# Performance work log

Measured on AMD Instinct MI355X. Metric: run time of the kernel, lower is better.

Reference implementation:

```python
import jax, jax.numpy as jnp
import numpy as np

D_IN = 1024
D_OUT = 1024
NUM_HEADS = 16
HEAD_DIM = D_OUT // NUM_HEADS
WINDOW = 256


def setup_inputs() -> dict:
    key = jax.random.key(0)
    ks = jax.random.split(key, 6)
    s = 0.02
    x = jax.random.normal(ks[0], (2, 2048, D_IN), dtype=jnp.float32)
    Wq = jax.random.normal(ks[1], (D_IN, D_OUT), dtype=jnp.float32) * s
    Wk = jax.random.normal(ks[2], (D_IN, D_OUT), dtype=jnp.float32) * s
    Wv = jax.random.normal(ks[3], (D_IN, D_OUT), dtype=jnp.float32) * s
    Wo = jax.random.normal(ks[4], (D_OUT, D_OUT), dtype=jnp.float32) * s
    bo = jnp.zeros((D_OUT,), dtype=jnp.float32)
    return {"x": x, "Wq": Wq, "Wk": Wk, "Wv": Wv, "Wo": Wo, "bo": bo}


def reference(x, Wq, Wk, Wv, Wo, bo):
    b, s, _ = x.shape
    # project and split heads: [b, h, s, hd]
    def heads(t):
        return t.reshape(b, s, NUM_HEADS, HEAD_DIM).transpose(0, 2, 1, 3)
    q = heads(x @ Wq)
    k = heads(x @ Wk)
    v = heads(x @ Wv)
    scores = jnp.einsum('bhqd,bhkd->bhqk', q, k) / jnp.sqrt(jnp.float32(HEAD_DIM))
    # symmetric sliding-window band: |i - j| <= WINDOW
    i = jnp.arange(s)
    band = jnp.abs(i[:, None] - i[None, :]) <= WINDOW  # [s, s]
    scores = jnp.where(band[None, None], scores, -jnp.inf)
    probs = jax.nn.softmax(scores, axis=-1)  # dropout=0.0 -> identity
    ctx = jnp.einsum('bhqk,bhkd->bhqd', probs, v)
    ctx = ctx.transpose(0, 2, 1, 3).reshape(b, s, D_OUT)
    return ctx @ Wo + bo
```

## Files before the change

kernel.cpp:

```cpp
#include <hip/hip_runtime.h>
#include <hip/hip_bf16.h>

typedef __bf16 bf16_t;
typedef __bf16 bf16x8 __attribute__((ext_vector_type(8)));
typedef __bf16 bf16x4 __attribute__((ext_vector_type(4)));
typedef float  f32x4  __attribute__((ext_vector_type(4)));

#define SEQ    2048
#define BATCH  2
#define NHEAD  16
#define HDIM   64
#define DMODEL 1024
#define WIN    256

__device__ __forceinline__ void async_load16(const void* g, void* l) {
    __builtin_amdgcn_global_load_lds(
        (const __attribute__((address_space(1))) char*)(uintptr_t)g,
        (__attribute__((address_space(3))) char*)(uintptr_t)l, 16, 0, 0);
}

__global__ void cast_x_kernel(const float* __restrict__ x, bf16_t* __restrict__ xb, int n4) {
    int i = blockIdx.x * blockDim.x + threadIdx.x;
    if (i >= n4) return;
    float4 v = ((const float4*)x)[i];
    bf16x4 o;
    o[0] = (bf16_t)v.x; o[1] = (bf16_t)v.y; o[2] = (bf16_t)v.z; o[3] = (bf16_t)v.w;
    ((bf16x4*)xb)[i] = o;
}

__global__ void transpose_w_kernel(const float* __restrict__ Wq, const float* __restrict__ Wk,
                                   const float* __restrict__ Wv, const float* __restrict__ Wo,
                                   bf16_t* __restrict__ Wt) {
    __shared__ float tile[32][33];
    const float* W = (blockIdx.z == 0) ? Wq : (blockIdx.z == 1) ? Wk : (blockIdx.z == 2) ? Wv : Wo;
    bf16_t* out = Wt + (size_t)blockIdx.z * DMODEL * DMODEL;
    int k0 = blockIdx.y * 32, n0 = blockIdx.x * 32;
    int tx = threadIdx.x, ty = threadIdx.y;
#pragma unroll
    for (int i = 0; i < 4; i++)
        tile[ty + i * 8][tx] = W[(size_t)(k0 + ty + i * 8) * DMODEL + n0 + tx];
    __syncthreads();
#pragma unroll
    for (int i = 0; i < 4; i++)
        out[(size_t)(n0 + ty + i * 8) * DMODEL + k0 + tx] = (bf16_t)tile[tx][ty + i * 8];
}

template <int EPI>
__global__ __launch_bounds__(256) void gemm_bt_kernel(
    const bf16_t* __restrict__ A, const bf16_t* __restrict__ Bt,
    bf16_t* __restrict__ Qb, bf16_t* __restrict__ Kb, bf16_t* __restrict__ Vt,
    float* __restrict__ Out, const float* __restrict__ bo, int K) {
    __shared__ __attribute__((aligned(16))) bf16_t As[128 * 64];
    __shared__ __attribute__((aligned(16))) bf16_t Bs[128 * 64];
    const int tid = threadIdx.x;
    const int wave = tid >> 6, lane = tid & 63, quad = lane >> 4, l15 = lane & 15;
    const int wm = wave >> 1, wn = wave & 1;
    const int m0 = blockIdx.y * 128, n0 = blockIdx.x * 128;

    f32x4 acc[4][4] = {};

    for (int kt = 0; kt < K; kt += 64) {
#pragma unroll
        for (int i = 0; i < 4; i++) {
            int v = tid + i * 256;
            int row = v >> 3, c = (v & 7) ^ (row & 7);
            async_load16(A + (size_t)(m0 + row) * K + kt + c * 8, (char*)As + (size_t)v * 16);
            async_load16(Bt + (size_t)(n0 + row) * K + kt + c * 8, (char*)Bs + (size_t)v * 16);
        }
        __syncthreads();
#pragma unroll
        for (int kk = 0; kk < 64; kk += 32) {
            bf16x8 am[4], bn[4];
#pragma unroll
            for (int i = 0; i < 4; i++) {
                int row = wm * 64 + i * 16 + l15;
                int ch = ((kk >> 3) + quad) ^ (row & 7);
                am[i] = *(const bf16x8*)&As[row * 64 + ch * 8];
            }
#pragma unroll
            for (int j = 0; j < 4; j++) {
                int row = wn * 64 + j * 16 + l15;
                int ch = ((kk >> 3) + quad) ^ (row & 7);
                bn[j] = *(const bf16x8*)&Bs[row * 64 + ch * 8];
            }
#pragma unroll
            for (int i = 0; i < 4; i++)
#pragma unroll
                for (int j = 0; j < 4; j++)
                    acc[i][j] = __builtin_amdgcn_mfma_f32_16x16x32_bf16(am[i], bn[j], acc[i][j], 0, 0, 0);
        }
        __syncthreads();
    }

#pragma unroll
    for (int i = 0; i < 4; i++)
#pragma unroll
        for (int j = 0; j < 4; j++)
#pragma unroll
            for (int r = 0; r < 4; r++) {
                int mg = m0 + wm * 64 + i * 16 + quad * 4 + r;
                int ng = n0 + wn * 64 + j * 16 + l15;
                float v = acc[i][j][r];
                if (EPI == 0) {
                    int sel = ng >> 10, nl = ng & 1023, h = nl >> 6, d = nl & 63;
                    int b = mg >> 11, s = mg & 2047;
                    size_t idx = ((size_t)((b * NHEAD + h) * SEQ) + s) * HDIM + d;
                    if (sel == 0)      Qb[idx] = (bf16_t)(v * 0.125f);
                    else if (sel == 1) Kb[idx] = (bf16_t)v;
                    else               Vt[((size_t)((b * NHEAD + h) * HDIM) + d) * SEQ + s] = (bf16_t)v;
                } else {
                    Out[(size_t)mg * DMODEL + ng] = v + bo[ng];
                }
            }
}

__global__ __launch_bounds__(256) void attn_kernel(
    const bf16_t* __restrict__ Qb, const bf16_t* __restrict__ Kb,
    const bf16_t* __restrict__ Vt, bf16_t* __restrict__ ctx) {
    __shared__ __attribute__((aligned(16))) bf16_t Ks[2][64 * 64];
    __shared__ __attribute__((aligned(16))) bf16_t Vs[2][64 * 64];
    __shared__ __attribute__((aligned(16))) bf16_t Plds[4][16][72];
    const int tid = threadIdx.x;
    const int wave = tid >> 6, lane = tid & 63, quad = lane >> 4, l15 = lane & 15;

    const int id = blockIdx.x;
    const int task = (id & 7) * 128 + (id >> 3);
    const int b = task >> 9, h = (task >> 5) & 15, q0 = (task & 31) << 6;
    const int qbase = q0 + wave * 16;

    const bf16_t* Qp = Qb + (size_t)(b * NHEAD + h) * SEQ * HDIM;
    const bf16_t* Kp = Kb + (size_t)(b * NHEAD + h) * SEQ * HDIM;
    const bf16_t* Vp = Vt + (size_t)(b * NHEAD + h) * HDIM * SEQ;

    bf16x8 qa0 = *(const bf16x8*)(Qp + (size_t)(qbase + l15) * HDIM + quad * 8);
    bf16x8 qa1 = *(const bf16x8*)(Qp + (size_t)(qbase + l15) * HDIM + 32 + quad * 8);

    bf16x8 ones;
#pragma unroll
    for (int j = 0; j < 8; j++) ones[j] = (bf16_t)1.0f;

    f32x4 O[4] = {};
    f32x4 lacc = {};

    const int qt = q0 >> 6;
    const int t0 = (qt - 4 > 0) ? qt - 4 : 0;
    const int t1 = (qt + 4 < SEQ / 64 - 1) ? qt + 4 : SEQ / 64 - 1;

    auto stage = [&](int kt, int buf) {
        const int k0 = kt * 64;
#pragma unroll
        for (int i = 0; i < 2; i++) {
            int v = tid + i * 256;
            int row = v >> 3, c = (v & 7) ^ (row & 7);
            async_load16(Kp + (size_t)(k0 + row) * HDIM + c * 8, (char*)&Ks[buf][0] + (size_t)v * 16);
            async_load16(Vp + (size_t)row * SEQ + k0 + c * 8, (char*)&Vs[buf][0] + (size_t)v * 16);
        }
    };

    stage(t0, 0);
    int cb = 0;
    for (int kt = t0; kt <= t1; kt++) {
        __syncthreads();
        if (kt < t1) stage(kt + 1, cb ^ 1);
        const int k0 = kt * 64;
        f32x4 s[4];
#pragma unroll
        for (int c = 0; c < 4; c++) {
            int row = c * 16 + l15;
            bf16x8 kb0 = *(const bf16x8*)&Ks[cb][row * 64 + (quad ^ (row & 7)) * 8];
            bf16x8 kb1 = *(const bf16x8*)&Ks[cb][row * 64 + ((quad + 4) ^ (row & 7)) * 8];
            f32x4 a = {};
            a = __builtin_amdgcn_mfma_f32_16x16x32_bf16(qa0, kb0, a, 0, 0, 0);
            a = __builtin_amdgcn_mfma_f32_16x16x32_bf16(qa1, kb1, a, 0, 0, 0);
            s[c] = a;
        }
        const int dt = kt - qt;
        const bool edge = (dt <= -4 || dt >= 4);
#pragma unroll
        for (int c = 0; c < 4; c++)
#pragma unroll
            for (int r = 0; r < 4; r++) {
                float sv = s[c][r];
                if (edge) {
                    int i = qbase + quad * 4 + r;
                    int j = k0 + c * 16 + l15;
                    int dd = i - j; dd = (dd < 0) ? -dd : dd;
                    if (dd > WIN) sv = -1e30f;
                }
                Plds[wave][quad * 4 + r][c * 16 + l15] = (bf16_t)__expf(sv);
            }
        bf16x8 pa0 = *(const bf16x8*)&Plds[wave][l15][quad * 8];
        bf16x8 pa1 = *(const bf16x8*)&Plds[wave][l15][32 + quad * 8];
        lacc = __builtin_amdgcn_mfma_f32_16x16x32_bf16(pa0, ones, lacc, 0, 0, 0);
        lacc = __builtin_amdgcn_mfma_f32_16x16x32_bf16(pa1, ones, lacc, 0, 0, 0);
#pragma unroll
        for (int d = 0; d < 4; d++) {
            int row = d * 16 + l15;
            bf16x8 vb0 = *(const bf16x8*)&Vs[cb][row * 64 + (quad ^ (row & 7)) * 8];
            bf16x8 vb1 = *(const bf16x8*)&Vs[cb][row * 64 + ((quad + 4) ^ (row & 7)) * 8];
            O[d] = __builtin_amdgcn_mfma_f32_16x16x32_bf16(pa0, vb0, O[d], 0, 0, 0);
            O[d] = __builtin_amdgcn_mfma_f32_16x16x32_bf16(pa1, vb1, O[d], 0, 0, 0);
        }
        __syncthreads();
        cb ^= 1;
    }

#pragma unroll
    for (int r = 0; r < 4; r++) {
        float inv = 1.0f / lacc[r];
        int i = qbase + quad * 4 + r;
#pragma unroll
        for (int d = 0; d < 4; d++) {
            float v = O[d][r] * inv;
            ctx[((size_t)(b * SEQ + i)) * DMODEL + h * HDIM + d * 16 + l15] = (bf16_t)v;
        }
    }
}

extern "C" void kernel_launch(void* const* d_in, const int* in_sizes, int n_in,
                              void* d_out, int out_size, void* d_ws, size_t ws_size,
                              hipStream_t stream) {
    const float* x  = (const float*)d_in[0];
    const float* Wq = (const float*)d_in[1];
    const float* Wk = (const float*)d_in[2];
    const float* Wv = (const float*)d_in[3];
    const float* Wo = (const float*)d_in[4];
    const float* bo = (const float*)d_in[5];
    float* out = (float*)d_out;

    const size_t MTOK = (size_t)BATCH * SEQ;
    bf16_t* xb  = (bf16_t*)d_ws;
    bf16_t* Wt  = xb + MTOK * DMODEL;
    bf16_t* Qb  = Wt + (size_t)4 * DMODEL * DMODEL;
    bf16_t* Kb  = Qb + MTOK * DMODEL;
    bf16_t* Vt  = Kb + MTOK * DMODEL;
    bf16_t* ctx = Vt + MTOK * DMODEL;

    cast_x_kernel<<<dim3((MTOK * DMODEL / 4 + 255) / 256), dim3(256), 0, stream>>>(
        x, xb, (int)(MTOK * DMODEL / 4));
    transpose_w_kernel<<<dim3(32, 32, 4), dim3(32, 8), 0, stream>>>(Wq, Wk, Wv, Wo, Wt);
    gemm_bt_kernel<0><<<dim3(24, 32), dim3(256), 0, stream>>>(
        xb, Wt, Qb, Kb, Vt, nullptr, nullptr, DMODEL);
    attn_kernel<<<dim3(1024), dim3(256), 0, stream>>>(Qb, Kb, Vt, ctx);
    gemm_bt_kernel<1><<<dim3(8, 32), dim3(256), 0, stream>>>(
        ctx, Wt + (size_t)3 * DMODEL * DMODEL, nullptr, nullptr, nullptr, out, bo, DMODEL);
}
```

Before: 179.0 us.

## Share K/V tiles across 128-query blocks, separate V transpose, XCD-aware GEMM tiling

The attention kernel now runs 512 threads (8 waves) over 128 queries, so each staged 64-key K/V tile serves two query tiles. This cuts redundant K/V global loads; waves skip tiles outside their own band. The QKV GEMM now writes V in row layout, and a new kernel transposes it into Vt, replacing the scattered strided stores in the GEMM epilogue. GEMM block indices are remapped so each XCD owns a contiguous set of N columns for L2 locality, at the cost of an extra launch and extra V traffic.

```diff
diff --git a/kernel.cpp b/kernel.cpp
--- a/kernel.cpp
+++ b/kernel.cpp
@@ -45,17 +45,38 @@
         out[(size_t)(n0 + ty + i * 8) * DMODEL + k0 + tx] = (bf16_t)tile[tx][ty + i * 8];
 }
 
+__global__ __launch_bounds__(256) void vtrans_kernel(const bf16_t* __restrict__ Vb,
+                                                     bf16_t* __restrict__ Vt) {
+    __shared__ bf16_t tile[64][65];
+    const int bh = blockIdx.y, s0 = blockIdx.x * 64;
+    const int tx = threadIdx.x, ty = threadIdx.y;
+    const bf16_t* src = Vb + ((size_t)bh * SEQ + s0) * HDIM;
+    bf16_t* dst = Vt + (size_t)bh * HDIM * SEQ + s0;
+#pragma unroll
+    for (int i = 0; i < 16; i++) {
+        int row = i * 4 + ty;
+        tile[row][tx] = src[(size_t)row * HDIM + tx];
+    }
+    __syncthreads();
+#pragma unroll
+    for (int i = 0; i < 16; i++) {
+        int d = i * 4 + ty;
+        dst[(size_t)d * SEQ + tx] = tile[tx][d];
+    }
+}
+
 template <int EPI>
 __global__ __launch_bounds__(256) void gemm_bt_kernel(
     const bf16_t* __restrict__ A, const bf16_t* __restrict__ Bt,
-    bf16_t* __restrict__ Qb, bf16_t* __restrict__ Kb, bf16_t* __restrict__ Vt,
-    float* __restrict__ Out, const float* __restrict__ bo, int K) {
+    bf16_t* __restrict__ Qb, bf16_t* __restrict__ Kb, bf16_t* __restrict__ Vb,
+    float* __restrict__ Out, const float* __restrict__ bo, int K, int nPer) {
     __shared__ __attribute__((aligned(16))) bf16_t As[128 * 64];
     __shared__ __attribute__((aligned(16))) bf16_t Bs[128 * 64];
     const int tid = threadIdx.x;
     const int wave = tid >> 6, lane = tid & 63, quad = lane >> 4, l15 = lane & 15;
     const int wm = wave >> 1, wn = wave & 1;
-    const int m0 = blockIdx.y * 128, n0 = blockIdx.x * 128;
+    const int id = blockIdx.x, xcd = id & 7, t = id >> 3;
+    const int m0 = (t / nPer) * 128, n0 = (xcd * nPer + t % nPer) * 128;
 
     f32x4 acc[4][4] = {};
 
@@ -107,26 +128,27 @@
                     size_t idx = ((size_t)((b * NHEAD + h) * SEQ) + s) * HDIM + d;
                     if (sel == 0)      Qb[idx] = (bf16_t)(v * 0.125f);
                     else if (sel == 1) Kb[idx] = (bf16_t)v;
-                    else               Vt[((size_t)((b * NHEAD + h) * HDIM) + d) * SEQ + s] = (bf16_t)v;
+                    else               Vb[idx] = (bf16_t)v;
                 } else {
                     Out[(size_t)mg * DMODEL + ng] = v + bo[ng];
                 }
             }
 }
 
-__global__ __launch_bounds__(256) void attn_kernel(
+__global__ __launch_bounds__(512) void attn_kernel(
     const bf16_t* __restrict__ Qb, const bf16_t* __restrict__ Kb,
     const bf16_t* __restrict__ Vt, bf16_t* __restrict__ ctx) {
     __shared__ __attribute__((aligned(16))) bf16_t Ks[2][64 * 64];
     __shared__ __attribute__((aligned(16))) bf16_t Vs[2][64 * 64];
-    __shared__ __attribute__((aligned(16))) bf16_t Plds[4][16][72];
+    __shared__ __attribute__((aligned(16))) bf16_t Plds[8][16][72];
     const int tid = threadIdx.x;
     const int wave = tid >> 6, lane = tid & 63, quad = lane >> 4, l15 = lane & 15;
 
     const int id = blockIdx.x;
-    const int task = (id & 7) * 128 + (id >> 3);
-    const int b = task >> 9, h = (task >> 5) & 15, q0 = (task & 31) << 6;
-    const int qbase = q0 + wave * 16;
+    const int task = (id & 7) * 64 + (id >> 3);
+    const int b = task >> 8, h = (task >> 4) & 15, Q0 = (task & 15) << 7;
+    const int qbase = Q0 + wave * 16;
+    const int wqt = (Q0 >> 6) + (wave >> 2);
 
     const bf16_t* Qp = Qb + (size_t)(b * NHEAD + h) * SEQ * HDIM;
     const bf16_t* Kp = Kb + (size_t)(b * NHEAD + h) * SEQ * HDIM;
@@ -142,64 +164,63 @@
     f32x4 O[4] = {};
     f32x4 lacc = {};
 
-    const int qt = q0 >> 6;
-    const int t0 = (qt - 4 > 0) ? qt - 4 : 0;
-    const int t1 = (qt + 4 < SEQ / 64 - 1) ? qt + 4 : SEQ / 64 - 1;
+    const int base_t = Q0 >> 6;
+    const int bt0 = (base_t - 4 > 0) ? base_t - 4 : 0;
+    const int bt1 = (base_t + 5 < SEQ / 64 - 1) ? base_t + 5 : SEQ / 64 - 1;
 
     auto stage = [&](int kt, int buf) {
         const int k0 = kt * 64;
-#pragma unroll
-        for (int i = 0; i < 2; i++) {
-            int v = tid + i * 256;
-            int row = v >> 3, c = (v & 7) ^ (row & 7);
-            async_load16(Kp + (size_t)(k0 + row) * HDIM + c * 8, (char*)&Ks[buf][0] + (size_t)v * 16);
-            async_load16(Vp + (size_t)row * SEQ + k0 + c * 8, (char*)&Vs[buf][0] + (size_t)v * 16);
-        }
+        int v = tid;
+        int row = v >> 3, c = (v & 7) ^ (row & 7);
+        async_load16(Kp + (size_t)(k0 + row) * HDIM + c * 8, (char*)&Ks[buf][0] + (size_t)v * 16);
+        async_load16(Vp + (size_t)row * SEQ + k0 + c * 8, (char*)&Vs[buf][0] + (size_t)v * 16);
     };
 
-    stage(t0, 0);
+    stage(bt0, 0);
     int cb = 0;
-    for (int kt = t0; kt <= t1; kt++) {
-        __syncthreads();
-        if (kt < t1) stage(kt + 1, cb ^ 1);
-        const int k0 = kt * 64;
-        f32x4 s[4];
-#pragma unroll
-        for (int c = 0; c < 4; c++) {
-            int row = c * 16 + l15;
-            bf16x8 kb0 = *(const bf16x8*)&Ks[cb][row * 64 + (quad ^ (row & 7)) * 8];
-            bf16x8 kb1 = *(const bf16x8*)&Ks[cb][row * 64 + ((quad + 4) ^ (row & 7)) * 8];
-            f32x4 a = {};
-            a = __builtin_amdgcn_mfma_f32_16x16x32_bf16(qa0, kb0, a, 0, 0, 0);
-            a = __builtin_amdgcn_mfma_f32_16x16x32_bf16(qa1, kb1, a, 0, 0, 0);
-            s[c] = a;
-        }
-        const int dt = kt - qt;
-        const bool edge = (dt <= -4 || dt >= 4);
-#pragma unroll
-        for (int c = 0; c < 4; c++)
-#pragma unroll
-            for (int r = 0; r < 4; r++) {
-                float sv = s[c][r];
-                if (edge) {
-                    int i = qbase + quad * 4 + r;
-                    int j = k0 + c * 16 + l15;
-                    int dd = i - j; dd = (dd < 0) ? -dd : dd;
-                    if (dd > WIN) sv = -1e30f;
+    for (int kt = bt0; kt <= bt1; kt++) {
+        __syncthreads();
+        if (kt < bt1) stage(kt + 1, cb ^ 1);
+        const int dt = kt - wqt;
+        if (dt >= -4 && dt <= 4) {
+            const int k0 = kt * 64;
+            f32x4 s[4];
+#pragma unroll
+            for (int c = 0; c < 4; c++) {
+                int row = c * 16 + l15;
+                bf16x8 kb0 = *(const bf16x8*)&Ks[cb][row * 64 + (quad ^ (row & 7)) * 8];
+                bf16x8 kb1 = *(const bf16x8*)&Ks[cb][row * 64 + ((quad + 4) ^ (row & 7)) * 8];
+                f32x4 a = {};
+                a = __builtin_amdgcn_mfma_f32_16x16x32_bf16(qa0, kb0, a, 0, 0, 0);
+                a = __builtin_amdgcn_mfma_f32_16x16x32_bf16(qa1, kb1, a, 0, 0, 0);
+                s[c] = a;
+            }
+            const bool edge = (dt == -4 || dt == 4);
+#pragma unroll
+            for (int c = 0; c < 4; c++)
+#pragma unroll
+                for (int r = 0; r < 4; r++) {
+                    float sv = s[c][r];
+                    if (edge) {
+                        int i = qbase + quad * 4 + r;
+                        int j = k0 + c * 16 + l15;
+                        int dd = i - j; dd = (dd < 0) ? -dd : dd;
+                        if (dd > WIN) sv = -1e30f;
+                    }
+                    Plds[wave][quad * 4 + r][c * 16 + l15] = (bf16_t)__expf(sv);
                 }
-                Plds[wave][quad * 4 + r][c * 16 + l15] = (bf16_t)__expf(sv);
-            }
-        bf16x8 pa0 = *(const bf16x8*)&Plds[wave][l15][quad * 8];
-        bf16x8 pa1 = *(const bf16x8*)&Plds[wave][l15][32 + quad * 8];
-        lacc = __builtin_amdgcn_mfma_f32_16x16x32_bf16(pa0, ones, lacc, 0, 0, 0);
-        lacc = __builtin_amdgcn_mfma_f32_16x16x32_bf16(pa1, ones, lacc, 0, 0, 0);
-#pragma unroll
-        for (int d = 0; d < 4; d++) {
-            int row = d * 16 + l15;
-            bf16x8 vb0 = *(const bf16x8*)&Vs[cb][row * 64 + (quad ^ (row & 7)) * 8];
-            bf16x8 vb1 = *(const bf16x8*)&Vs[cb][row * 64 + ((quad + 4) ^ (row & 7)) * 8];
-            O[d] = __builtin_amdgcn_mfma_f32_16x16x32_bf16(pa0, vb0, O[d], 0, 0, 0);
-            O[d] = __builtin_amdgcn_mfma_f32_16x16x32_bf16(pa1, vb1, O[d], 0, 0, 0);
+            bf16x8 pa0 = *(const bf16x8*)&Plds[wave][l15][quad * 8];
+            bf16x8 pa1 = *(const bf16x8*)&Plds[wave][l15][32 + quad * 8];
+            lacc = __builtin_amdgcn_mfma_f32_16x16x32_bf16(pa0, ones, lacc, 0, 0, 0);
+            lacc = __builtin_amdgcn_mfma_f32_16x16x32_bf16(pa1, ones, lacc, 0, 0, 0);
+#pragma unroll
+            for (int d = 0; d < 4; d++) {
+                int row = d * 16 + l15;
+                bf16x8 vb0 = *(const bf16x8*)&Vs[cb][row * 64 + (quad ^ (row & 7)) * 8];
+                bf16x8 vb1 = *(const bf16x8*)&Vs[cb][row * 64 + ((quad + 4) ^ (row & 7)) * 8];
+                O[d] = __builtin_amdgcn_mfma_f32_16x16x32_bf16(pa0, vb0, O[d], 0, 0, 0);
+                O[d] = __builtin_amdgcn_mfma_f32_16x16x32_bf16(pa1, vb1, O[d], 0, 0, 0);
+            }
         }
         __syncthreads();
         cb ^= 1;
@@ -235,13 +256,15 @@
     bf16_t* Kb  = Qb + MTOK * DMODEL;
     bf16_t* Vt  = Kb + MTOK * DMODEL;
     bf16_t* ctx = Vt + MTOK * DMODEL;
+    bf16_t* Vb  = ctx;
 
     cast_x_kernel<<<dim3((MTOK * DMODEL / 4 + 255) / 256), dim3(256), 0, stream>>>(
         x, xb, (int)(MTOK * DMODEL / 4));
     transpose_w_kernel<<<dim3(32, 32, 4), dim3(32, 8), 0, stream>>>(Wq, Wk, Wv, Wo, Wt);
-    gemm_bt_kernel<0><<<dim3(24, 32), dim3(256), 0, stream>>>(
-        xb, Wt, Qb, Kb, Vt, nullptr, nullptr, DMODEL);
-    attn_kernel<<<dim3(1024), dim3(256), 0, stream>>>(Qb, Kb, Vt, ctx);
-    gemm_bt_kernel<1><<<dim3(8, 32), dim3(256), 0, stream>>>(
-        ctx, Wt + (size_t)3 * DMODEL * DMODEL, nullptr, nullptr, nullptr, out, bo, DMODEL);
-}
+    gemm_bt_kernel<0><<<dim3(768), dim3(256), 0, stream>>>(
+        xb, Wt, Qb, Kb, Vb, nullptr, nullptr, DMODEL, 3);
+    vtrans_kernel<<<dim3(32, 32), dim3(64, 4), 0, stream>>>(Vb, Vt);
+    attn_kernel<<<dim3(512), dim3(512), 0, stream>>>(Qb, Kb, Vt, ctx);
+    gemm_bt_kernel<1><<<dim3(256), dim3(256), 0, stream>>>(
+        ctx, Wt + (size_t)3 * DMODEL * DMODEL, nullptr, nullptr, nullptr, out, bo, DMODEL, 1);
+}
```

Result: faster. 170.4 us (-4.8%).
